# Kernel tuning notes

Measured on AMD Instinct MI355X. Metric: run time of the kernel, lower is better.

## Reference

```python
import jax, jax.numpy as jnp
import numpy as np

T, D, H = 32768, 64, 128  # timesteps, input_size, hidden_size

def setup_inputs() -> dict:
    key = jax.random.key(0)
    ks = jax.random.split(key, 13)
    s_ih = 1.0 / np.sqrt(H)
    def u(k, shape):
        return jax.random.uniform(k, shape, jnp.float32, -s_ih, s_ih)
    return {
        "X": jax.random.normal(ks[0], (T, 1, D), jnp.float32),
        "W_ih": u(ks[1], (4 * H, D)),
        "W_hh": u(ks[2], (4 * H, H)),
        "b_ih": u(ks[3], (4 * H,)),
        "b_hh": u(ks[4], (4 * H,)),
        "W1": u(ks[5], (11, H)), "b1": u(ks[6], (11,)),
        "W2": u(ks[7], (2, H)),  "b2": u(ks[8], (2,)),
        "W3": u(ks[9], (1, H)),  "b3": u(ks[10], (1,)),
        "W4": u(ks[11], (1, H)), "b4": u(ks[12], (1,)),
    }

def reference(X, W_ih, W_hh, b_ih, b_hh, W1, b1, W2, b2, W3, b3, W4, b4):
    # LSTMCell recurrence over T steps, batch=1 (masks are identity: Dropout(p=0) on ones)
    def cell(carry, x):
        h, c = carry  # [1,H]
        gates = x @ W_ih.T + b_ih + h @ W_hh.T + b_hh  # [1,4H]
        i, f, g, o = jnp.split(gates, 4, axis=-1)
        c2 = jax.nn.sigmoid(f) * c + jax.nn.sigmoid(i) * jnp.tanh(g)
        h2 = jax.nn.sigmoid(o) * jnp.tanh(c2)
        return (h2, c2), h2

    h0 = jnp.zeros((1, H), X.dtype)
    c0 = jnp.zeros((1, H), X.dtype)
    _, hs = jax.lax.scan(cell, (h0, c0), X)  # hs: [T,1,H]
    out = hs[:, 0, :]  # squeeze -> [T,H]

    # MtFc head: 4 small linears on the same features
    step = out @ W1.T + b1        # [T,11]
    experience = out @ W2.T + b2  # [T,2]
    rsd = out @ W3.T + b3         # [T,1]
    s = out @ W4.T + b4           # [T,1]
    return (step, experience, rsd, s)
```

## Files before the change

kernel.cpp:

```cpp
#include <hip/hip_runtime.h>
#include <hip/hip_bf16.h>
#include <cstdint>
#include <cstddef>

#define T_STEPS 32768
#define DD 64
#define HH 128
#define GG 512

#define OFF_EXP 360448
#define OFF_RSD 425984
#define OFF_S   458752

typedef __attribute__((ext_vector_type(8))) _Float16 half8;
typedef __attribute__((ext_vector_type(4))) float f32x4;

__device__ __forceinline__ float exp2_f(float x) {
    float r; asm("v_exp_f32 %0, %1" : "=v"(r) : "v"(x)); return r;
}
__device__ __forceinline__ float sigm_fast(float x) {
    return __builtin_amdgcn_rcpf(1.0f + exp2_f(x * -1.442695041f));
}
__device__ __forceinline__ float tanh_fast(float x) {
    return __builtin_fmaf(
        __builtin_amdgcn_rcpf(1.0f + exp2_f(x * 2.885390082f)), -2.0f, 1.0f);
}

__global__ __launch_bounds__(512, 2) void pregate_kernel(
    const float* __restrict__ X, const float* __restrict__ W_ih,
    const float* __restrict__ b_ih, const float* __restrict__ b_hh,
    float* __restrict__ P, int t0, int nrows)
{
    __shared__ __align__(16) float xs[DD];
    const int j = threadIdx.x;
    const int grow = (j & 3) * HH + (j >> 2);

    float w[DD];
    const float4* wv = reinterpret_cast<const float4*>(W_ih + (size_t)grow * DD);
#pragma unroll
    for (int k = 0; k < DD / 4; ++k) {
        float4 v = wv[k];
        w[4*k+0] = v.x; w[4*k+1] = v.y; w[4*k+2] = v.z; w[4*k+3] = v.w;
    }
    const float bias = b_ih[grow] + b_hh[grow];

    const int rpb = (nrows + gridDim.x - 1) / gridDim.x;
    const int r0  = blockIdx.x * rpb;
    const int r1  = (r0 + rpb < nrows) ? (r0 + rpb) : nrows;

    for (int r = r0; r < r1; ++r) {
        const int t = t0 + r;
        if (j < DD) xs[j] = X[(size_t)t * DD + j];
        __syncthreads();
        float acc = bias;
        const float4* xv = reinterpret_cast<const float4*>(xs);
#pragma unroll
        for (int k = 0; k < DD / 4; ++k) {
            float4 v = xv[k];
            acc += v.x*w[4*k+0] + v.y*w[4*k+1] + v.z*w[4*k+2] + v.w*w[4*k+3];
        }
        P[(size_t)r * GG + j] = acc;
        __syncthreads();
    }
}

__global__ __launch_bounds__(256, 1) void lstm_seq_kernel(
    const float* __restrict__ P, const float* __restrict__ W_hh,
    float* __restrict__ hist, float* __restrict__ state,
    int t0, int C)
{
    __shared__ __align__(16) _Float16 hh2[2][HH];

    const int j    = threadIdx.x;
    const int w    = j >> 6;
    const int l    = j & 63;
    const int col  = l & 15;
    const int kgrp = l >> 4;
    const int blk  = kgrp >> 1;
    const int mycell = 32 * w + 16 * blk + col;
    const bool pubH  = (kgrp & 1) == 0;
    const bool pubHist = (kgrp & 1) == 1;

    half8 wf[2][4][4];
#pragma unroll
    for (int s = 0; s < 2; ++s) {
#pragma unroll
        for (int mt = 0; mt < 4; ++mt) {
            const float* wr =
                W_hh + (size_t)(mt * HH + 32 * w + 16 * s + col) * HH + 8 * kgrp;
#pragma unroll
            for (int kt = 0; kt < 4; ++kt) {
                const float* wp = wr + 32 * kt;
                float4 w0 = *reinterpret_cast<const float4*>(wp);
                float4 w1 = *reinterpret_cast<const float4*>(wp + 4);
                half8 hf;
                hf[0] = (_Float16)w0.x; hf[1] = (_Float16)w0.y;
                hf[2] = (_Float16)w0.z; hf[3] = (_Float16)w0.w;
                hf[4] = (_Float16)w1.x; hf[5] = (_Float16)w1.y;
                hf[6] = (_Float16)w1.z; hf[7] = (_Float16)w1.w;
                wf[s][mt][kt] = hf;
            }
        }
    }

    float c = 0.0f;
    if (t0 != 0) c = state[HH + mycell];
    if (j < HH) hh2[0][j] = (_Float16)((t0 != 0) ? state[j] : 0.0f);
    __syncthreads();

    const float* Pme = P + 4 * (size_t)mycell;
    const f32x4 Z = {0.0f, 0.0f, 0.0f, 0.0f};
    f32x4 pc  = *reinterpret_cast<const f32x4*>(Pme);
    f32x4 pn1 = (C > 1) ? *reinterpret_cast<const f32x4*>(Pme + GG) : Z;
    float hn = 0.0f;

#pragma unroll 1
    for (int r = 0; r < C; ++r) {
        const _Float16* hb = &hh2[r & 1][8 * kgrp];
        const half8 a0 = *reinterpret_cast<const half8*>(hb);
        const half8 a1 = *reinterpret_cast<const half8*>(hb + 32);
        const half8 a2 = *reinterpret_cast<const half8*>(hb + 64);
        const half8 a3 = *reinterpret_cast<const half8*>(hb + 96);

        f32x4 pn2 = Z;
        if (r + 2 < C) pn2 = *reinterpret_cast<const f32x4*>(Pme + (size_t)(r + 2) * GG);

        f32x4 qa0, qa1, qa2, qa3, qb0, qb1, qb2, qb3;
#define MF(A, B, Cc) __builtin_amdgcn_mfma_f32_16x16x32_f16((A), (B), (Cc), 0, 0, 0)
        qa0 = MF(a0, wf[0][0][0], Z); qa1 = MF(a0, wf[0][1][0], Z);
        qa2 = MF(a0, wf[0][2][0], Z); qa3 = MF(a0, wf[0][3][0], Z);
        qb0 = MF(a0, wf[1][0][0], Z); qb1 = MF(a0, wf[1][1][0], Z);
        qb2 = MF(a0, wf[1][2][0], Z); qb3 = MF(a0, wf[1][3][0], Z);

        qa0 = MF(a1, wf[0][0][1], qa0); qa1 = MF(a1, wf[0][1][1], qa1);
        qa2 = MF(a1, wf[0][2][1], qa2); qa3 = MF(a1, wf[0][3][1], qa3);
        qb0 = MF(a1, wf[1][0][1], qb0); qb1 = MF(a1, wf[1][1][1], qb1);
        qb2 = MF(a1, wf[1][2][1], qb2); qb3 = MF(a1, wf[1][3][1], qb3);

        qa0 = MF(a2, wf[0][0][2], qa0); qa1 = MF(a2, wf[0][1][2], qa1);
        qa2 = MF(a2, wf[0][2][2], qa2); qa3 = MF(a2, wf[0][3][2], qa3);
        qb0 = MF(a2, wf[1][0][2], qb0); qb1 = MF(a2, wf[1][1][2], qb1);
        qb2 = MF(a2, wf[1][2][2], qb2); qb3 = MF(a2, wf[1][3][2], qb3);

        qa0 = MF(a3, wf[0][0][3], qa0); qa1 = MF(a3, wf[0][1][3], qa1);
        qa2 = MF(a3, wf[0][2][3], qa2); qa3 = MF(a3, wf[0][3][3], qa3);
        qb0 = MF(a3, wf[1][0][3], qb0); qb1 = MF(a3, wf[1][1][3], qb1);
        qb2 = MF(a3, wf[1][2][3], qb2); qb3 = MF(a3, wf[1][3][3], qb3);
#undef MF

        const bool useB = (blk != 0);
        const float si = useB ? qb0[0] : qa0[0];
        const float sf = useB ? qb1[0] : qa1[0];
        const float sg = useB ? qb2[0] : qa2[0];
        const float so = useB ? qb3[0] : qa3[0];

        const float ai = sigm_fast(si + pc[0]);
        const float af = sigm_fast(sf + pc[1]);
        const float ag = tanh_fast(sg + pc[2]);
        const float ao = sigm_fast(so + pc[3]);
        c = __builtin_fmaf(af, c, ai * ag);
        hn = ao * tanh_fast(c);

        if (pubH)         hh2[(r & 1) ^ 1][mycell] = (_Float16)hn;
        else if (pubHist) hist[(size_t)r * HH + mycell] = hn;

        pc = pn1; pn1 = pn2;

        asm volatile("s_waitcnt lgkmcnt(0)" ::: "memory");
        __builtin_amdgcn_s_barrier();
        __builtin_amdgcn_sched_barrier(0);
    }

    if (pubH) {
        state[mycell]      = hn;
        state[HH + mycell] = c;
    }
}

__global__ __launch_bounds__(256, 4) void heads_kernel(
    const float* __restrict__ hist,
    const float* __restrict__ W1, const float* __restrict__ b1,
    const float* __restrict__ W2, const float* __restrict__ b2,
    const float* __restrict__ W3, const float* __restrict__ b3,
    const float* __restrict__ W4, const float* __restrict__ b4,
    float* __restrict__ out, int t0, int C)
{
    const int idx = blockIdx.x * 256 + threadIdx.x;
    const int tr  = idx >> 4;
    const int oi  = idx & 15;
    if (tr >= C || oi >= 15) return;

    const float* wrow;
    float bias;
    if (oi < 11)       { wrow = W1 + oi * HH;        bias = b1[oi]; }
    else if (oi < 13)  { wrow = W2 + (oi - 11) * HH; bias = b2[oi - 11]; }
    else if (oi == 13) { wrow = W3;                  bias = b3[0]; }
    else               { wrow = W4;                  bias = b4[0]; }

    const float4* h4 = reinterpret_cast<const float4*>(hist + (size_t)tr * HH);
    const float4* w4 = reinterpret_cast<const float4*>(wrow);
    float s = bias;
#pragma unroll
    for (int k = 0; k < HH / 4; ++k) {
        float4 hv = h4[k];
        float4 wv = w4[k];
        s += hv.x*wv.x + hv.y*wv.y + hv.z*wv.z + hv.w*wv.w;
    }
    const int t = t0 + tr;
    if (oi < 11)       out[(size_t)t * 11 + oi] = s;
    else if (oi < 13)  out[OFF_EXP + (size_t)t * 2 + (oi - 11)] = s;
    else if (oi == 13) out[OFF_RSD + t] = s;
    else               out[OFF_S + t] = s;
}

extern "C" void kernel_launch(void* const* d_in, const int* in_sizes, int n_in,
                              void* d_out, int out_size, void* d_ws, size_t ws_size,
                              hipStream_t stream)
{
    const float* X    = (const float*)d_in[0];
    const float* W_ih = (const float*)d_in[1];
    const float* W_hh = (const float*)d_in[2];
    const float* b_ih = (const float*)d_in[3];
    const float* b_hh = (const float*)d_in[4];
    const float* W1   = (const float*)d_in[5];
    const float* b1   = (const float*)d_in[6];
    const float* W2   = (const float*)d_in[7];
    const float* b2   = (const float*)d_in[8];
    const float* W3   = (const float*)d_in[9];
    const float* b3   = (const float*)d_in[10];
    const float* W4   = (const float*)d_in[11];
    const float* b4   = (const float*)d_in[12];

    float* out   = (float*)d_out;
    float* state = (float*)d_ws;

    size_t avail = (ws_size > 1024) ? (ws_size - 1024) / 2560 : 0;
    int C = (avail >= (size_t)T_STEPS) ? T_STEPS : (int)avail;
    if (C < 1) C = 1;
    float* hist = state + 256;
    float* P    = hist + (size_t)C * HH;

    for (int t0 = 0; t0 < T_STEPS; t0 += C) {
        const int Cc = (C < T_STEPS - t0) ? C : (T_STEPS - t0);
        const int nb = (Cc < 512) ? Cc : 512;
        pregate_kernel<<<nb, 512, 0, stream>>>(X, W_ih, b_ih, b_hh, P, t0, Cc);
        lstm_seq_kernel<<<1, 256, 0, stream>>>(P, W_hh, hist, state, t0, Cc);
        heads_kernel<<<(Cc * 16 + 255) / 256, 256, 0, stream>>>(
            hist, W1, b1, W2, b2, W3, b3, W4, b4, out, t0, Cc);
    }
}
```

Measured before the change: 17.43 ms.

## Split recurrent matvec between MFMA and VALU dot2 to shorten per-step chain

The recurrent h·W_hh product is split along K. The first 64 inputs still go through the MFMA chain, now two k-tiles deep instead of four. The last 64 are computed per cell on the VALU with packed fp16 v_dot2 instructions, using W_hh slices held in registers. A ds_swizzle then adds the two lane halves together. The aim is to shorten the serial dependency chain of each timestep by running matrix and vector units in parallel, at the cost of extra VALU instructions and a cross-lane reduction step.

```diff
diff --git a/kernel.cpp b/kernel.cpp
--- a/kernel.cpp
+++ b/kernel.cpp
@@ -15,6 +15,9 @@
 typedef __attribute__((ext_vector_type(8))) _Float16 half8;
 typedef __attribute__((ext_vector_type(4))) float f32x4;
 
+__device__ __forceinline__ int   f2i(float x) { union { float f; int i; } u; u.f = x; return u.i; }
+__device__ __forceinline__ float i2f(int x)   { union { int i; float f; } u; u.i = x; return u.f; }
+
 __device__ __forceinline__ float exp2_f(float x) {
     float r; asm("v_exp_f32 %0, %1" : "=v"(r) : "v"(x)); return r;
 }
@@ -25,6 +28,13 @@
     return __builtin_fmaf(
         __builtin_amdgcn_rcpf(1.0f + exp2_f(x * 2.885390082f)), -2.0f, 1.0f);
 }
+__device__ __forceinline__ unsigned packh2(float x, float y) {
+    union { _Float16 h[2]; unsigned u; } c;
+    c.h[0] = (_Float16)x; c.h[1] = (_Float16)y;
+    return c.u;
+}
+#define D2(acc, wreg, hreg) \
+    asm("v_dot2_f32_f16 %0, %1, %2, %0" : "+v"(acc) : "v"(wreg), "v"(hreg))
 
 __global__ __launch_bounds__(512, 2) void pregate_kernel(
     const float* __restrict__ X, const float* __restrict__ W_ih,
@@ -71,17 +81,16 @@
 {
     __shared__ __align__(16) _Float16 hh2[2][HH];
 
-    const int j    = threadIdx.x;
-    const int w    = j >> 6;
-    const int l    = j & 63;
-    const int col  = l & 15;
-    const int kgrp = l >> 4;
-    const int blk  = kgrp >> 1;
+    const int j     = threadIdx.x;
+    const int w     = j >> 6;
+    const int l     = j & 63;
+    const int col   = l & 15;
+    const int kgrp  = l >> 4;
+    const int blk   = kgrp >> 1;
+    const int khalf = kgrp & 1;
     const int mycell = 32 * w + 16 * blk + col;
-    const bool pubH  = (kgrp & 1) == 0;
-    const bool pubHist = (kgrp & 1) == 1;
-
-    half8 wf[2][4][4];
+
+    half8 wf[2][4][2];
 #pragma unroll
     for (int s = 0; s < 2; ++s) {
 #pragma unroll
@@ -89,7 +98,7 @@
             const float* wr =
                 W_hh + (size_t)(mt * HH + 32 * w + 16 * s + col) * HH + 8 * kgrp;
 #pragma unroll
-            for (int kt = 0; kt < 4; ++kt) {
+            for (int kt = 0; kt < 2; ++kt) {
                 const float* wp = wr + 32 * kt;
                 float4 w0 = *reinterpret_cast<const float4*>(wp);
                 float4 w1 = *reinterpret_cast<const float4*>(wp + 4);
@@ -103,6 +112,15 @@
         }
     }
 
+    unsigned vw[4][16];
+#pragma unroll
+    for (int g = 0; g < 4; ++g) {
+        const float* wr = W_hh + (size_t)(g * HH + mycell) * HH + 64 + 32 * khalf;
+#pragma unroll
+        for (int k = 0; k < 16; ++k)
+            vw[g][k] = packh2(wr[2*k], wr[2*k+1]);
+    }
+
     float c = 0.0f;
     if (t0 != 0) c = state[HH + mycell];
     if (j < HH) hh2[0][j] = (_Float16)((t0 != 0) ? state[j] : 0.0f);
@@ -116,53 +134,59 @@
 
 #pragma unroll 1
     for (int r = 0; r < C; ++r) {
-        const _Float16* hb = &hh2[r & 1][8 * kgrp];
+        const int cur = r & 1;
+        const _Float16* hb = &hh2[cur][8 * kgrp];
         const half8 a0 = *reinterpret_cast<const half8*>(hb);
         const half8 a1 = *reinterpret_cast<const half8*>(hb + 32);
-        const half8 a2 = *reinterpret_cast<const half8*>(hb + 64);
-        const half8 a3 = *reinterpret_cast<const half8*>(hb + 96);
+        const uint4* hvp = reinterpret_cast<const uint4*>(&hh2[cur][64 + 32 * khalf]);
+        const uint4 hv0 = hvp[0], hv1 = hvp[1], hv2 = hvp[2], hv3 = hvp[3];
 
         f32x4 pn2 = Z;
         if (r + 2 < C) pn2 = *reinterpret_cast<const f32x4*>(Pme + (size_t)(r + 2) * GG);
 
-        f32x4 qa0, qa1, qa2, qa3, qb0, qb1, qb2, qb3;
 #define MF(A, B, Cc) __builtin_amdgcn_mfma_f32_16x16x32_f16((A), (B), (Cc), 0, 0, 0)
-        qa0 = MF(a0, wf[0][0][0], Z); qa1 = MF(a0, wf[0][1][0], Z);
-        qa2 = MF(a0, wf[0][2][0], Z); qa3 = MF(a0, wf[0][3][0], Z);
-        qb0 = MF(a0, wf[1][0][0], Z); qb1 = MF(a0, wf[1][1][0], Z);
-        qb2 = MF(a0, wf[1][2][0], Z); qb3 = MF(a0, wf[1][3][0], Z);
-
+        f32x4 qa0 = MF(a0, wf[0][0][0], Z); f32x4 qa1 = MF(a0, wf[0][1][0], Z);
+        f32x4 qa2 = MF(a0, wf[0][2][0], Z); f32x4 qa3 = MF(a0, wf[0][3][0], Z);
+        f32x4 qb0 = MF(a0, wf[1][0][0], Z); f32x4 qb1 = MF(a0, wf[1][1][0], Z);
+        f32x4 qb2 = MF(a0, wf[1][2][0], Z); f32x4 qb3 = MF(a0, wf[1][3][0], Z);
+
+        float d0 = 0.f, d1 = 0.f, d2 = 0.f, d3 = 0.f;
+#define DP(hreg) { D2(d0, vw[0][kk], hreg); D2(d1, vw[1][kk], hreg); \
+                   D2(d2, vw[2][kk], hreg); D2(d3, vw[3][kk], hreg); ++kk; }
+        {
+            int kk = 0;
+            DP(hv0.x) DP(hv0.y) DP(hv0.z) DP(hv0.w)
+            DP(hv1.x) DP(hv1.y) DP(hv1.z) DP(hv1.w)
+            DP(hv2.x) DP(hv2.y) DP(hv2.z) DP(hv2.w)
+            DP(hv3.x) DP(hv3.y) DP(hv3.z) DP(hv3.w)
+        }
+#undef DP
         qa0 = MF(a1, wf[0][0][1], qa0); qa1 = MF(a1, wf[0][1][1], qa1);
         qa2 = MF(a1, wf[0][2][1], qa2); qa3 = MF(a1, wf[0][3][1], qa3);
         qb0 = MF(a1, wf[1][0][1], qb0); qb1 = MF(a1, wf[1][1][1], qb1);
         qb2 = MF(a1, wf[1][2][1], qb2); qb3 = MF(a1, wf[1][3][1], qb3);
-
-        qa0 = MF(a2, wf[0][0][2], qa0); qa1 = MF(a2, wf[0][1][2], qa1);
-        qa2 = MF(a2, wf[0][2][2], qa2); qa3 = MF(a2, wf[0][3][2], qa3);
-        qb0 = MF(a2, wf[1][0][2], qb0); qb1 = MF(a2, wf[1][1][2], qb1);
-        qb2 = MF(a2, wf[1][2][2], qb2); qb3 = MF(a2, wf[1][3][2], qb3);
-
-        qa0 = MF(a3, wf[0][0][3], qa0); qa1 = MF(a3, wf[0][1][3], qa1);
-        qa2 = MF(a3, wf[0][2][3], qa2); qa3 = MF(a3, wf[0][3][3], qa3);
-        qb0 = MF(a3, wf[1][0][3], qb0); qb1 = MF(a3, wf[1][1][3], qb1);
-        qb2 = MF(a3, wf[1][2][3], qb2); qb3 = MF(a3, wf[1][3][3], qb3);
 #undef MF
 
+        d0 += i2f(__builtin_amdgcn_ds_swizzle(f2i(d0), 0x401F));
+        d1 += i2f(__builtin_amdgcn_ds_swizzle(f2i(d1), 0x401F));
+        d2 += i2f(__builtin_amdgcn_ds_swizzle(f2i(d2), 0x401F));
+        d3 += i2f(__builtin_amdgcn_ds_swizzle(f2i(d3), 0x401F));
+
         const bool useB = (blk != 0);
-        const float si = useB ? qb0[0] : qa0[0];
-        const float sf = useB ? qb1[0] : qa1[0];
-        const float sg = useB ? qb2[0] : qa2[0];
-        const float so = useB ? qb3[0] : qa3[0];
-
-        const float ai = sigm_fast(si + pc[0]);
-        const float af = sigm_fast(sf + pc[1]);
-        const float ag = tanh_fast(sg + pc[2]);
-        const float ao = sigm_fast(so + pc[3]);
+        const float si = (useB ? qb0[0] : qa0[0]) + d0 + pc[0];
+        const float sf = (useB ? qb1[0] : qa1[0]) + d1 + pc[1];
+        const float sg = (useB ? qb2[0] : qa2[0]) + d2 + pc[2];
+        const float so = (useB ? qb3[0] : qa3[0]) + d3 + pc[3];
+
+        const float ai = sigm_fast(si);
+        const float af = sigm_fast(sf);
+        const float ag = tanh_fast(sg);
+        const float ao = sigm_fast(so);
         c = __builtin_fmaf(af, c, ai * ag);
         hn = ao * tanh_fast(c);
 
-        if (pubH)         hh2[(r & 1) ^ 1][mycell] = (_Float16)hn;
-        else if (pubHist) hist[(size_t)r * HH + mycell] = hn;
+        if (khalf == 0) hh2[cur ^ 1][mycell] = (_Float16)hn;
+        else            hist[(size_t)r * HH + mycell] = hn;
 
         pc = pn1; pn1 = pn2;
 
@@ -171,7 +195,7 @@
         __builtin_amdgcn_sched_barrier(0);
     }
 
-    if (pubH) {
+    if (khalf == 0) {
         state[mycell]      = hn;
         state[HH + mycell] = c;
     }
```

After: 20.83 ms. 1.2x slower.
